# Performance work log

Hardware: AMD Instinct MI355X
Metric: run time of the kernel (lower is better)

The kernel has to match this reference:

```python
import jax, jax.numpy as jnp
import numpy as np

E, K = 8, 2  # num_experts, top_k


def setup_inputs() -> dict:
    key = jax.random.key(0)
    ks = jax.random.split(key, 5)
    B, S, H, I = 2, 1024, 1024, 4096
    scale_h = 1.0 / np.sqrt(H)
    scale_i = 1.0 / np.sqrt(I)
    return {
        "hidden_states": jax.random.normal(ks[0], (B, S, H), jnp.float32),
        "conf_w": jax.random.normal(ks[1], (E, H), jnp.float32) * 0.1 * scale_h,
        "conf_b": jnp.zeros((E,), jnp.float32),
        "gate_w": jax.random.normal(ks[2], (E, I, H), jnp.float32) * scale_h,
        "up_w": jax.random.normal(ks[3], (E, I, H), jnp.float32) * scale_h,
        "down_w": jax.random.normal(ks[4], (E, H, I), jnp.float32) * scale_i,
        "wealth": jnp.ones((E,), jnp.float32),
    }


def reference(hidden_states, conf_w, conf_b, gate_w, up_w, down_w, wealth):
    x = hidden_states  # (B,S,H)
    # Per-expert confidence heads: sigmoid(Linear(H->1)) stacked -> (B,S,E)
    confidences = jax.nn.sigmoid(jnp.einsum("bsh,eh->bse", x, conf_w) + conf_b)
    # VCG auction: bid = confidence * wealth
    bids = confidences * wealth  # (B,S,E)
    top_bids, selected_experts = jax.lax.top_k(bids, K)  # (B,S,K)
    # payments = (K+1)-th highest bid (unused in output but part of forward math)
    sorted_bids = -jnp.sort(-bids, axis=-1)
    payments = jnp.broadcast_to(sorted_bids[..., K:K + 1], top_bids.shape)
    routing_weights = jax.nn.softmax(top_bids, axis=-1)  # (B,S,K)
    # combine weights per expert: sum_k rw_k * [sel_k == e] -> (B,S,E)
    combine = jnp.sum(
        jax.nn.one_hot(selected_experts, E, dtype=x.dtype)
        * routing_weights[..., None],
        axis=2,
    )

    def ffn(gw, uw, dw):
        # SwiGLU expert: down(silu(gate(x)) * up(x))
        g = jnp.einsum("bsh,ih->bsi", x, gw)
        u = jnp.einsum("bsh,ih->bsi", x, uw)
        return jnp.einsum("bsi,hi->bsh", jax.nn.silu(g) * u, dw)

    expert_out = jax.vmap(ffn)(gate_w, up_w, down_w)  # (E,B,S,H)
    output = jnp.einsum("ebsh,bse->bsh", expert_out, combine)
    return output
```

## Files before the change

### kernel.cpp

```cpp
#include <hip/hip_runtime.h>
#include <math.h>

#define NEXP 8
#define TILE 128
#define BK 32

typedef __attribute__((ext_vector_type(8))) short short8;
typedef __attribute__((ext_vector_type(4))) float float4v;

__device__ __forceinline__ unsigned short f2bf(float f) {
  union { float f; unsigned u; } v; v.f = f;
  unsigned r = v.u + 0x7FFFu + ((v.u >> 16) & 1u);
  return (unsigned short)(r >> 16);
}
__device__ __forceinline__ unsigned pack2(float a, float b) {
  return (unsigned)f2bf(a) | ((unsigned)f2bf(b) << 16);
}

__device__ __forceinline__ void gll16(const void* g, void* l) {
  __builtin_amdgcn_global_load_lds(
      (const __attribute__((address_space(1))) unsigned int*)(unsigned long long)(uintptr_t)g,
      (__attribute__((address_space(3))) unsigned int*)(unsigned)(uintptr_t)l,
      16, 0, 0);
}

__global__ __launch_bounds__(256) void convert_x_kernel(
    const float* __restrict__ x, unsigned short* __restrict__ xb, int n4) {
  int i = blockIdx.x * 256 + threadIdx.x;
  if (i >= n4) return;
  float4 v = ((const float4*)x)[i];
  uint2 o; o.x = pack2(v.x, v.y); o.y = pack2(v.z, v.w);
  ((uint2*)xb)[i] = o;
}

__global__ __launch_bounds__(256) void pack_w_kernel(
    const float* __restrict__ src, unsigned short* __restrict__ dst, int K) {
  const int ks = blockIdx.x, rt = blockIdx.y, e = blockIdx.z;
  const int n_ks = gridDim.x, n_rt = gridDim.y;
  const int r = threadIdx.x >> 1, half = threadIdx.x & 1;
  const size_t R = (size_t)n_rt * TILE;
  const float4* s = (const float4*)(src + ((size_t)e * R + rt * TILE + r) * K + ks * BK + half * 16);
  float4 v0 = s[0], v1 = s[1], v2 = s[2], v3 = s[3];
  uint4 o0, o1;
  o0.x = pack2(v0.x, v0.y); o0.y = pack2(v0.z, v0.w);
  o0.z = pack2(v1.x, v1.y); o0.w = pack2(v1.z, v1.w);
  o1.x = pack2(v2.x, v2.y); o1.y = pack2(v2.z, v2.w);
  o1.z = pack2(v3.x, v3.y); o1.w = pack2(v3.z, v3.w);
  unsigned short* pb = dst + ((size_t)(e * n_rt + rt) * n_ks + ks) * (TILE * BK)
                           + (r >> 4) * 512 + (r & 15) * 8;
  *(uint4*)(pb + (2 * half) * 128)     = o0;
  *(uint4*)(pb + (2 * half + 1) * 128) = o1;
}

__global__ __launch_bounds__(256) void routing_kernel(
    const float* __restrict__ x, const float* __restrict__ cw,
    const float* __restrict__ cb, const float* __restrict__ wealth,
    int* __restrict__ plist, int* __restrict__ counts,
    float* __restrict__ w_rt, int T, int H) {
  const int t = blockIdx.x;
  const int tid = threadIdx.x;
  const float* xr = x + (size_t)t * H;
  float acc[NEXP];
#pragma unroll
  for (int e = 0; e < NEXP; ++e) acc[e] = 0.f;
  for (int h = tid; h < H; h += 256) {
    float xv = xr[h];
#pragma unroll
    for (int e = 0; e < NEXP; ++e) acc[e] += xv * cw[e * H + h];
  }
  __shared__ float s[NEXP][256];
#pragma unroll
  for (int e = 0; e < NEXP; ++e) s[e][tid] = acc[e];
  __syncthreads();
  for (int st = 128; st > 0; st >>= 1) {
    if (tid < st) {
#pragma unroll
      for (int e = 0; e < NEXP; ++e) s[e][tid] += s[e][tid + st];
    }
    __syncthreads();
  }
  if (tid == 0) {
    float bids[NEXP];
#pragma unroll
    for (int e = 0; e < NEXP; ++e) {
      float lg = s[e][0] + cb[e];
      float c = 1.f / (1.f + expf(-lg));
      bids[e] = c * wealth[e];
    }
    int i0 = 0;
    for (int e = 1; e < NEXP; ++e) if (bids[e] > bids[i0]) i0 = e;
    int i1 = (i0 == 0) ? 1 : 0;
    for (int e = 0; e < NEXP; ++e) if (e != i0 && bids[e] > bids[i1]) i1 = e;
    float ex = expf(bids[i1] - bids[i0]);
    float wsum = 1.f + ex;
    w_rt[2 * t]     = 1.f / wsum;
    w_rt[2 * t + 1] = ex / wsum;
    int p0 = atomicAdd(&counts[i0], 1);
    plist[i0 * T + p0] = 2 * t;
    int p1 = atomicAdd(&counts[i1], 1);
    plist[i1 * T + p1] = 2 * t + 1;
  }
}

__global__ __launch_bounds__(256, 2) void gateup_kernel(
    const unsigned short* __restrict__ xb, const unsigned short* __restrict__ gwp,
    const unsigned short* __restrict__ uwp, const int* __restrict__ plist,
    const int* __restrict__ counts, unsigned short* __restrict__ act,
    int T, int H, int I) {
  const int nx = gridDim.x, ny = gridDim.y, nz = gridDim.z;
  int rt = blockIdx.x, it = blockIdx.y, e = blockIdx.z;
  {
    int nwg = nx * ny * nz;
    if (((nwg & 7) == 0) && (((nwg >> 3) % nx) == 0)) {
      int orig = blockIdx.x + nx * (blockIdx.y + ny * blockIdx.z);
      int idx = orig >> 3, xcd = orig & 7;
      int q = idx / nx;
      rt = idx - q * nx;
      int chunk = q * 8 + xcd;
      it = chunk % ny;
      e = chunk / ny;
    }
  }
  const int cnt = counts[e];
  const int row0 = rt * TILE;
  if (row0 >= cnt) return;
  const int nks = H / BK;

  __shared__ __align__(16) unsigned short As[2][TILE * BK];
  __shared__ __align__(16) unsigned short Bg[2][TILE * BK];
  __shared__ __align__(16) unsigned short Bu[2][TILE * BK];

  const int tid = threadIdx.x, lane = tid & 63, wv = tid >> 6;
  const int wm = wv >> 1, wn = wv & 1;
  const int quad = lane >> 4, l15 = lane & 15;

  int ri0 = row0 + wv * 32 + l15;
  int ri1 = ri0 + 16;
  if (ri0 >= cnt) ri0 = cnt - 1;
  if (ri1 >= cnt) ri1 = cnt - 1;
  const unsigned short* a0 = xb + (size_t)(plist[e * T + ri0] >> 1) * H + quad * 8;
  const unsigned short* a1 = xb + (size_t)(plist[e * T + ri1] >> 1) * H + quad * 8;

  const size_t pan = ((size_t)(e * ny + it) * nks) * (TILE * BK);
  const unsigned short* g0 = gwp + pan + (size_t)wv * 1024 + (size_t)lane * 8;
  const unsigned short* u0 = uwp + pan + (size_t)wv * 1024 + (size_t)lane * 8;

  float4v accg[4][4], accu[4][4];
#pragma unroll
  for (int a = 0; a < 4; ++a)
#pragma unroll
    for (int b = 0; b < 4; ++b) {
      float4v z = {0.f, 0.f, 0.f, 0.f};
      accg[a][b] = z; accu[a][b] = z;
    }

  auto stage = [&](int kk, int b) {
    unsigned short* lA = &As[b][wv * 1024];
    unsigned short* lG = &Bg[b][wv * 1024];
    unsigned short* lU = &Bu[b][wv * 1024];
    size_t ka = (size_t)kk * BK;
    size_t kb = (size_t)kk * (TILE * BK);
    gll16(a0 + ka, lA);       gll16(a1 + ka, lA + 512);
    gll16(g0 + kb, lG);       gll16(g0 + kb + 512, lG + 512);
    gll16(u0 + kb, lU);       gll16(u0 + kb + 512, lU + 512);
  };

  stage(0, 0);
  __syncthreads();
  for (int k = 0; k < nks; ++k) {
    const int cb = k & 1;
    if (k + 1 < nks) stage(k + 1, cb ^ 1);
    short8 af[4], bgf[4], buf_[4];
#pragma unroll
    for (int mi = 0; mi < 4; ++mi)
      af[mi] = *(const short8*)(&As[cb][(wm * 4 + mi) * 512 + quad * 128 + l15 * 8]);
#pragma unroll
    for (int ni = 0; ni < 4; ++ni) {
      bgf[ni]  = *(const short8*)(&Bg[cb][(wn * 4 + ni) * 512 + quad * 128 + l15 * 8]);
      buf_[ni] = *(const short8*)(&Bu[cb][(wn * 4 + ni) * 512 + quad * 128 + l15 * 8]);
    }
#pragma unroll
    for (int mi = 0; mi < 4; ++mi)
#pragma unroll
      for (int ni = 0; ni < 4; ++ni) {
        accg[mi][ni] = __builtin_amdgcn_mfma_f32_16x16x32_bf16(af[mi], bgf[ni], accg[mi][ni], 0, 0, 0);
        accu[mi][ni] = __builtin_amdgcn_mfma_f32_16x16x32_bf16(af[mi], buf_[ni], accu[mi][ni], 0, 0, 0);
      }
    __syncthreads();
  }

#pragma unroll
  for (int mi = 0; mi < 4; ++mi) {
    int rbase = wm * 64 + mi * 16 + quad * 4;
#pragma unroll
    for (int r = 0; r < 4; ++r) {
      int grow = row0 + rbase + r;
      if (grow < cnt) {
        int p = plist[e * T + grow];
        size_t base = (size_t)p * I + it * TILE + wn * 64 + l15;
#pragma unroll
        for (int ni = 0; ni < 4; ++ni) {
          float g = accg[mi][ni][r];
          float u = accu[mi][ni][r];
          float s = g / (1.f + __expf(-g)) * u;
          act[base + ni * 16] = f2bf(s);
        }
      }
    }
  }
}

__global__ __launch_bounds__(256, 2) void down_kernel(
    const unsigned short* __restrict__ act, const unsigned short* __restrict__ dwp,
    const int* __restrict__ plist, const int* __restrict__ counts,
    float* __restrict__ part, int T, int H, int I) {
  const int nx = gridDim.x, ny = gridDim.y, nz = gridDim.z;
  int rt = blockIdx.x, ht = blockIdx.y, zz = blockIdx.z;
  {
    int nwg = nx * ny * nz;
    if (((nwg & 7) == 0) && (((nwg >> 3) % nx) == 0)) {
      int orig = blockIdx.x + nx * (blockIdx.y + ny * blockIdx.z);
      int idx = orig >> 3, xcd = orig & 7;
      int q = idx / nx;
      rt = idx - q * nx;
      int chunk = q * 8 + xcd;
      ht = chunk % ny;
      zz = chunk / ny;
    }
  }
  const int e = zz >> 1, split = zz & 1;
  const int cnt = counts[e];
  const int row0 = rt * TILE;
  if (row0 >= cnt) return;
  const int nks_tot = I / BK;
  const int nks = nks_tot >> 1;
  const int k0 = split * nks;

  __shared__ __align__(16) unsigned short As[2][TILE * BK];
  __shared__ __align__(16) unsigned short Bs[2][TILE * BK];

  const int tid = threadIdx.x, lane = tid & 63, wv = tid >> 6;
  const int wm = wv >> 1, wn = wv & 1;
  const int quad = lane >> 4, l15 = lane & 15;

  int ri0 = row0 + wv * 32 + l15;
  int ri1 = ri0 + 16;
  if (ri0 >= cnt) ri0 = cnt - 1;
  if (ri1 >= cnt) ri1 = cnt - 1;
  const unsigned short* a0 = act + (size_t)plist[e * T + ri0] * I + k0 * BK + quad * 8;
  const unsigned short* a1 = act + (size_t)plist[e * T + ri1] * I + k0 * BK + quad * 8;

  const size_t pan = ((size_t)(e * ny + ht) * nks_tot + k0) * (TILE * BK);
  const unsigned short* b0 = dwp + pan + (size_t)wv * 1024 + (size_t)lane * 8;

  float4v acc[4][4];
#pragma unroll
  for (int a = 0; a < 4; ++a)
#pragma unroll
    for (int b = 0; b < 4; ++b) { float4v z = {0.f, 0.f, 0.f, 0.f}; acc[a][b] = z; }

  auto stage = [&](int kk, int b) {
    unsigned short* lA = &As[b][wv * 1024];
    unsigned short* lB = &Bs[b][wv * 1024];
    size_t ka = (size_t)kk * BK;
    size_t kb = (size_t)kk * (TILE * BK);
    gll16(a0 + ka, lA);  gll16(a1 + ka, lA + 512);
    gll16(b0 + kb, lB);  gll16(b0 + kb + 512, lB + 512);
  };

  stage(0, 0);
  __syncthreads();
  for (int k = 0; k < nks; ++k) {
    const int cb = k & 1;
    if (k + 1 < nks) stage(k + 1, cb ^ 1);
    short8 af[4], bf[4];
#pragma unroll
    for (int mi = 0; mi < 4; ++mi)
      af[mi] = *(const short8*)(&As[cb][(wm * 4 + mi) * 512 + quad * 128 + l15 * 8]);
#pragma unroll
    for (int ni = 0; ni < 4; ++ni)
      bf[ni] = *(const short8*)(&Bs[cb][(wn * 4 + ni) * 512 + quad * 128 + l15 * 8]);
#pragma unroll
    for (int mi = 0; mi < 4; ++mi)
#pragma unroll
      for (int ni = 0; ni < 4; ++ni)
        acc[mi][ni] = __builtin_amdgcn_mfma_f32_16x16x32_bf16(af[mi], bf[ni], acc[mi][ni], 0, 0, 0);
    __syncthreads();
  }

#pragma unroll
  for (int mi = 0; mi < 4; ++mi) {
    int rbase = wm * 64 + mi * 16 + quad * 4;
#pragma unroll
    for (int r = 0; r < 4; ++r) {
      int grow = row0 + rbase + r;
      if (grow < cnt) {
        int p = plist[e * T + grow];
        size_t base = ((size_t)split * 2 * T + p) * H + ht * TILE + wn * 64 + l15;
#pragma unroll
        for (int ni = 0; ni < 4; ++ni)
          part[base + ni * 16] = acc[mi][ni][r];
      }
    }
  }
}

__global__ __launch_bounds__(256) void combine_kernel(
    const float* __restrict__ part, const float* __restrict__ w_rt,
    float* __restrict__ out, int T, int H) {
  int h4 = H >> 2;
  int n4 = T * h4;
  int i = blockIdx.x * 256 + threadIdx.x;
  if (i >= n4) return;
  int t = i / h4;
  int c = i - t * h4;
  float w0 = w_rt[2 * t], w1 = w_rt[2 * t + 1];
  size_t splitoff = (size_t)2 * T * H / 4;
  const float4* pa = (const float4*)(part + (size_t)(2 * t) * H);
  const float4* pb = (const float4*)(part + (size_t)(2 * t + 1) * H);
  float4 a0 = pa[c], a1 = pa[c + splitoff];
  float4 b0 = pb[c], b1 = pb[c + splitoff];
  float4 o;
  o.x = w0 * (a0.x + a1.x) + w1 * (b0.x + b1.x);
  o.y = w0 * (a0.y + a1.y) + w1 * (b0.y + b1.y);
  o.z = w0 * (a0.z + a1.z) + w1 * (b0.z + b1.z);
  o.w = w0 * (a0.w + a1.w) + w1 * (b0.w + b1.w);
  ((float4*)(out + (size_t)t * H))[c] = o;
}

extern "C" void kernel_launch(void* const* d_in, const int* in_sizes, int n_in,
                              void* d_out, int out_size, void* d_ws, size_t ws_size,
                              hipStream_t stream) {
  const float* x      = (const float*)d_in[0];
  const float* cw     = (const float*)d_in[1];
  const float* cb     = (const float*)d_in[2];
  const float* gw     = (const float*)d_in[3];
  const float* uw     = (const float*)d_in[4];
  const float* dw     = (const float*)d_in[5];
  const float* wealth = (const float*)d_in[6];
  float* out = (float*)d_out;

  const int H = in_sizes[1] / NEXP;
  const int T = in_sizes[0] / H;
  const int I = in_sizes[3] / (NEXP * H);

  char* ws = (char*)d_ws;
  size_t off = 0;
  unsigned short* xb  = (unsigned short*)(ws + off); off += (size_t)T * H * 2;
  unsigned short* act = (unsigned short*)(ws + off); off += (size_t)2 * T * I * 2;
  float* part = (float*)(ws + off); off += (size_t)2 * 2 * T * H * 4;
  unsigned short* gwp = (unsigned short*)(ws + off); off += (size_t)NEXP * I * H * 2;
  unsigned short* uwp = (unsigned short*)(ws + off); off += (size_t)NEXP * I * H * 2;
  unsigned short* dwp = gwp;
  int* plist = (int*)(ws + off); off += (size_t)NEXP * T * 4;
  float* w_rt = (float*)(ws + off); off += (size_t)T * 2 * 4;
  int* counts = (int*)(ws + off); off += NEXP * 4;

  hipMemsetAsync(counts, 0, NEXP * sizeof(int), stream);

  int n4 = (T * H) / 4;
  convert_x_kernel<<<(n4 + 255) / 256, 256, 0, stream>>>(x, xb, n4);
  routing_kernel<<<T, 256, 0, stream>>>(x, cw, cb, wealth, plist, counts, w_rt, T, H);

  dim3 gp(H / BK, I / TILE, NEXP);
  pack_w_kernel<<<gp, 256, 0, stream>>>(gw, gwp, H);
  pack_w_kernel<<<gp, 256, 0, stream>>>(uw, uwp, H);

  int ttiles = (T + TILE - 1) / TILE;
  dim3 g1(ttiles, I / TILE, NEXP);
  gateup_kernel<<<g1, 256, 0, stream>>>(xb, gwp, uwp, plist, counts, act, T, H, I);

  dim3 gpd(I / BK, H / TILE, NEXP);
  pack_w_kernel<<<gpd, 256, 0, stream>>>(dw, dwp, I);

  dim3 g2(ttiles, H / TILE, NEXP * 2);
  down_kernel<<<g2, 256, 0, stream>>>(act, dwp, plist, counts, part, T, H, I);

  combine_kernel<<<(n4 + 255) / 256, 256, 0, stream>>>(part, w_rt, out, T, H);
}
```

Baseline: 692.6 us.

## Fuse fp32 weight conversion into GEMM loads and merge routing with x conversion

Removes the separate weight pack kernels. The gate/up and down GEMMs now read fp32 weights directly into registers, convert them with v_cvt_pk_bf16_f32, and write them into LDS in the MFMA layout, with the register prefetch overlapping the MFMA work. The x conversion and the routing are merged into one launch, and routing uses one wave per token with shuffle reductions. The gain is fewer passes over the weights and fewer launches. In exchange each GEMM tile re-reads fp32 weights (twice the bytes) once per token tile, adds register pressure, and down_kernel's launch bound rises to 3 blocks.

```diff
diff --git a/kernel.cpp b/kernel.cpp
--- a/kernel.cpp
+++ b/kernel.cpp
@@ -15,6 +15,17 @@
 }
 __device__ __forceinline__ unsigned pack2(float a, float b) {
   return (unsigned)f2bf(a) | ((unsigned)f2bf(b) << 16);
+}
+__device__ __forceinline__ unsigned cvtpk(float lo, float hi) {
+  unsigned r;
+  asm("v_cvt_pk_bf16_f32 %0, %1, %2" : "=v"(r) : "v"(lo), "v"(hi));
+  return r;
+}
+__device__ __forceinline__ uint4 cvt8(float4 a, float4 b) {
+  uint4 o;
+  o.x = cvtpk(a.x, a.y); o.y = cvtpk(a.z, a.w);
+  o.z = cvtpk(b.x, b.y); o.w = cvtpk(b.z, b.w);
+  return o;
 }
 
 __device__ __forceinline__ void gll16(const void* g, void* l) {
@@ -24,66 +35,51 @@
       16, 0, 0);
 }
 
-__global__ __launch_bounds__(256) void convert_x_kernel(
-    const float* __restrict__ x, unsigned short* __restrict__ xb, int n4) {
-  int i = blockIdx.x * 256 + threadIdx.x;
-  if (i >= n4) return;
-  float4 v = ((const float4*)x)[i];
-  uint2 o; o.x = pack2(v.x, v.y); o.y = pack2(v.z, v.w);
-  ((uint2*)xb)[i] = o;
-}
-
-__global__ __launch_bounds__(256) void pack_w_kernel(
-    const float* __restrict__ src, unsigned short* __restrict__ dst, int K) {
-  const int ks = blockIdx.x, rt = blockIdx.y, e = blockIdx.z;
-  const int n_ks = gridDim.x, n_rt = gridDim.y;
-  const int r = threadIdx.x >> 1, half = threadIdx.x & 1;
-  const size_t R = (size_t)n_rt * TILE;
-  const float4* s = (const float4*)(src + ((size_t)e * R + rt * TILE + r) * K + ks * BK + half * 16);
-  float4 v0 = s[0], v1 = s[1], v2 = s[2], v3 = s[3];
-  uint4 o0, o1;
-  o0.x = pack2(v0.x, v0.y); o0.y = pack2(v0.z, v0.w);
-  o0.z = pack2(v1.x, v1.y); o0.w = pack2(v1.z, v1.w);
-  o1.x = pack2(v2.x, v2.y); o1.y = pack2(v2.z, v2.w);
-  o1.z = pack2(v3.x, v3.y); o1.w = pack2(v3.z, v3.w);
-  unsigned short* pb = dst + ((size_t)(e * n_rt + rt) * n_ks + ks) * (TILE * BK)
-                           + (r >> 4) * 512 + (r & 15) * 8;
-  *(uint4*)(pb + (2 * half) * 128)     = o0;
-  *(uint4*)(pb + (2 * half + 1) * 128) = o1;
-}
-
-__global__ __launch_bounds__(256) void routing_kernel(
+__global__ __launch_bounds__(256) void prep_kernel(
     const float* __restrict__ x, const float* __restrict__ cw,
     const float* __restrict__ cb, const float* __restrict__ wealth,
-    int* __restrict__ plist, int* __restrict__ counts,
-    float* __restrict__ w_rt, int T, int H) {
-  const int t = blockIdx.x;
-  const int tid = threadIdx.x;
-  const float* xr = x + (size_t)t * H;
+    unsigned short* __restrict__ xb, int* __restrict__ plist,
+    int* __restrict__ counts, float* __restrict__ w_rt,
+    int T, int H, int n4, int nconv) {
+  const int b = blockIdx.x;
+  if (b < nconv) {
+    int i = b * 256 + threadIdx.x;
+    if (i < n4) {
+      float4 v = ((const float4*)x)[i];
+      uint2 o; o.x = pack2(v.x, v.y); o.y = pack2(v.z, v.w);
+      ((uint2*)xb)[i] = o;
+    }
+    return;
+  }
+  int t = (b - nconv) * 4 + (threadIdx.x >> 6);
+  if (t >= T) return;
+  const int lane = threadIdx.x & 63;
+  const float4* x4 = (const float4*)(x + (size_t)t * H);
+  const float4* c4 = (const float4*)cw;
+  const int h4n = H >> 2;
   float acc[NEXP];
 #pragma unroll
   for (int e = 0; e < NEXP; ++e) acc[e] = 0.f;
-  for (int h = tid; h < H; h += 256) {
-    float xv = xr[h];
-#pragma unroll
-    for (int e = 0; e < NEXP; ++e) acc[e] += xv * cw[e * H + h];
-  }
-  __shared__ float s[NEXP][256];
-#pragma unroll
-  for (int e = 0; e < NEXP; ++e) s[e][tid] = acc[e];
-  __syncthreads();
-  for (int st = 128; st > 0; st >>= 1) {
-    if (tid < st) {
-#pragma unroll
-      for (int e = 0; e < NEXP; ++e) s[e][tid] += s[e][tid + st];
-    }
-    __syncthreads();
-  }
-  if (tid == 0) {
+  for (int h = lane; h < h4n; h += 64) {
+    float4 xv = x4[h];
+#pragma unroll
+    for (int e = 0; e < NEXP; ++e) {
+      float4 cv = c4[(size_t)e * h4n + h];
+      acc[e] += xv.x * cv.x + xv.y * cv.y + xv.z * cv.z + xv.w * cv.w;
+    }
+  }
+#pragma unroll
+  for (int e = 0; e < NEXP; ++e) {
+    float v = acc[e];
+#pragma unroll
+    for (int off = 32; off > 0; off >>= 1) v += __shfl_down(v, off, 64);
+    acc[e] = v;
+  }
+  if (lane == 0) {
     float bids[NEXP];
 #pragma unroll
     for (int e = 0; e < NEXP; ++e) {
-      float lg = s[e][0] + cb[e];
+      float lg = acc[e] + cb[e];
       float c = 1.f / (1.f + expf(-lg));
       bids[e] = c * wealth[e];
     }
@@ -103,8 +99,8 @@
 }
 
 __global__ __launch_bounds__(256, 2) void gateup_kernel(
-    const unsigned short* __restrict__ xb, const unsigned short* __restrict__ gwp,
-    const unsigned short* __restrict__ uwp, const int* __restrict__ plist,
+    const unsigned short* __restrict__ xb, const float* __restrict__ gw,
+    const float* __restrict__ uw, const int* __restrict__ plist,
     const int* __restrict__ counts, unsigned short* __restrict__ act,
     int T, int H, int I) {
   const int nx = gridDim.x, ny = gridDim.y, nz = gridDim.z;
@@ -141,9 +137,11 @@
   const unsigned short* a0 = xb + (size_t)(plist[e * T + ri0] >> 1) * H + quad * 8;
   const unsigned short* a1 = xb + (size_t)(plist[e * T + ri1] >> 1) * H + quad * 8;
 
-  const size_t pan = ((size_t)(e * ny + it) * nks) * (TILE * BK);
-  const unsigned short* g0 = gwp + pan + (size_t)wv * 1024 + (size_t)lane * 8;
-  const unsigned short* u0 = uwp + pan + (size_t)wv * 1024 + (size_t)lane * 8;
+  const int brow = wv * 32 + (lane >> 1);
+  const int bhalf = lane & 1;
+  const float* gsrc = gw + ((size_t)e * I + (size_t)it * TILE + brow) * H + bhalf * 16;
+  const float* usrc = uw + ((size_t)e * I + (size_t)it * TILE + brow) * H + bhalf * 16;
+  const int woff = (brow >> 4) * 512 + bhalf * 256 + (brow & 15) * 8;
 
   float4v accg[4][4], accu[4][4];
 #pragma unroll
@@ -154,22 +152,34 @@
       accg[a][b] = z; accu[a][b] = z;
     }
 
-  auto stage = [&](int kk, int b) {
-    unsigned short* lA = &As[b][wv * 1024];
-    unsigned short* lG = &Bg[b][wv * 1024];
-    unsigned short* lU = &Bu[b][wv * 1024];
-    size_t ka = (size_t)kk * BK;
-    size_t kb = (size_t)kk * (TILE * BK);
-    gll16(a0 + ka, lA);       gll16(a1 + ka, lA + 512);
-    gll16(g0 + kb, lG);       gll16(g0 + kb + 512, lG + 512);
-    gll16(u0 + kb, lU);       gll16(u0 + kb + 512, lU + 512);
-  };
-
-  stage(0, 0);
+  float4 gr0, gr1, gr2, gr3, ur0, ur1, ur2, ur3;
+  auto loadB = [&](int kk) {
+    const float4* gs = (const float4*)(gsrc + (size_t)kk * BK);
+    const float4* us = (const float4*)(usrc + (size_t)kk * BK);
+    gr0 = gs[0]; gr1 = gs[1]; gr2 = gs[2]; gr3 = gs[3];
+    ur0 = us[0]; ur1 = us[1]; ur2 = us[2]; ur3 = us[3];
+  };
+  auto writeB = [&](int b) {
+    uint4 q0 = cvt8(gr0, gr1), q1 = cvt8(gr2, gr3);
+    uint4 q2 = cvt8(ur0, ur1), q3 = cvt8(ur2, ur3);
+    *(uint4*)(&Bg[b][woff])       = q0;
+    *(uint4*)(&Bg[b][woff + 128]) = q1;
+    *(uint4*)(&Bu[b][woff])       = q2;
+    *(uint4*)(&Bu[b][woff + 128]) = q3;
+  };
+  auto stageA = [&](int kk, int b) {
+    gll16(a0 + (size_t)kk * BK, &As[b][wv * 1024]);
+    gll16(a1 + (size_t)kk * BK, &As[b][wv * 1024 + 512]);
+  };
+
+  loadB(0);
+  stageA(0, 0);
+  writeB(0);
   __syncthreads();
+
   for (int k = 0; k < nks; ++k) {
     const int cb = k & 1;
-    if (k + 1 < nks) stage(k + 1, cb ^ 1);
+    if (k + 1 < nks) { loadB(k + 1); stageA(k + 1, cb ^ 1); }
     short8 af[4], bgf[4], buf_[4];
 #pragma unroll
     for (int mi = 0; mi < 4; ++mi)
@@ -186,6 +196,7 @@
         accg[mi][ni] = __builtin_amdgcn_mfma_f32_16x16x32_bf16(af[mi], bgf[ni], accg[mi][ni], 0, 0, 0);
         accu[mi][ni] = __builtin_amdgcn_mfma_f32_16x16x32_bf16(af[mi], buf_[ni], accu[mi][ni], 0, 0, 0);
       }
+    if (k + 1 < nks) writeB(cb ^ 1);
     __syncthreads();
   }
 
@@ -210,8 +221,8 @@
   }
 }
 
-__global__ __launch_bounds__(256, 2) void down_kernel(
-    const unsigned short* __restrict__ act, const unsigned short* __restrict__ dwp,
+__global__ __launch_bounds__(256, 3) void down_kernel(
+    const unsigned short* __restrict__ act, const float* __restrict__ dw,
     const int* __restrict__ plist, const int* __restrict__ counts,
     float* __restrict__ part, int T, int H, int I) {
   const int nx = gridDim.x, ny = gridDim.y, nz = gridDim.z;
@@ -250,8 +261,10 @@
   const unsigned short* a0 = act + (size_t)plist[e * T + ri0] * I + k0 * BK + quad * 8;
   const unsigned short* a1 = act + (size_t)plist[e * T + ri1] * I + k0 * BK + quad * 8;
 
-  const size_t pan = ((size_t)(e * ny + ht) * nks_tot + k0) * (TILE * BK);
-  const unsigned short* b0 = dwp + pan + (size_t)wv * 1024 + (size_t)lane * 8;
+  const int brow = wv * 32 + (lane >> 1);
+  const int bhalf = lane & 1;
+  const float* dsrc = dw + ((size_t)e * H + (size_t)ht * TILE + brow) * I + k0 * BK + bhalf * 16;
+  const int woff = (brow >> 4) * 512 + bhalf * 256 + (brow & 15) * 8;
 
   float4v acc[4][4];
 #pragma unroll
@@ -259,20 +272,29 @@
 #pragma unroll
     for (int b = 0; b < 4; ++b) { float4v z = {0.f, 0.f, 0.f, 0.f}; acc[a][b] = z; }
 
-  auto stage = [&](int kk, int b) {
-    unsigned short* lA = &As[b][wv * 1024];
-    unsigned short* lB = &Bs[b][wv * 1024];
-    size_t ka = (size_t)kk * BK;
-    size_t kb = (size_t)kk * (TILE * BK);
-    gll16(a0 + ka, lA);  gll16(a1 + ka, lA + 512);
-    gll16(b0 + kb, lB);  gll16(b0 + kb + 512, lB + 512);
-  };
-
-  stage(0, 0);
+  float4 dr0, dr1, dr2, dr3;
+  auto loadB = [&](int kk) {
+    const float4* ds = (const float4*)(dsrc + (size_t)kk * BK);
+    dr0 = ds[0]; dr1 = ds[1]; dr2 = ds[2]; dr3 = ds[3];
+  };
+  auto writeB = [&](int b) {
+    uint4 q0 = cvt8(dr0, dr1), q1 = cvt8(dr2, dr3);
+    *(uint4*)(&Bs[b][woff])       = q0;
+    *(uint4*)(&Bs[b][woff + 128]) = q1;
+  };
+  auto stageA = [&](int kk, int b) {
+    gll16(a0 + (size_t)kk * BK, &As[b][wv * 1024]);
+    gll16(a1 + (size_t)kk * BK, &As[b][wv * 1024 + 512]);
+  };
+
+  loadB(0);
+  stageA(0, 0);
+  writeB(0);
   __syncthreads();
+
   for (int k = 0; k < nks; ++k) {
     const int cb = k & 1;
-    if (k + 1 < nks) stage(k + 1, cb ^ 1);
+    if (k + 1 < nks) { loadB(k + 1); stageA(k + 1, cb ^ 1); }
     short8 af[4], bf[4];
 #pragma unroll
     for (int mi = 0; mi < 4; ++mi)
@@ -285,6 +307,7 @@
 #pragma unroll
       for (int ni = 0; ni < 4; ++ni)
         acc[mi][ni] = __builtin_amdgcn_mfma_f32_16x16x32_bf16(af[mi], bf[ni], acc[mi][ni], 0, 0, 0);
+    if (k + 1 < nks) writeB(cb ^ 1);
     __syncthreads();
   }
 
@@ -349,9 +372,6 @@
   unsigned short* xb  = (unsigned short*)(ws + off); off += (size_t)T * H * 2;
   unsigned short* act = (unsigned short*)(ws + off); off += (size_t)2 * T * I * 2;
   float* part = (float*)(ws + off); off += (size_t)2 * 2 * T * H * 4;
-  unsigned short* gwp = (unsigned short*)(ws + off); off += (size_t)NEXP * I * H * 2;
-  unsigned short* uwp = (unsigned short*)(ws + off); off += (size_t)NEXP * I * H * 2;
-  unsigned short* dwp = gwp;
   int* plist = (int*)(ws + off); off += (size_t)NEXP * T * 4;
   float* w_rt = (float*)(ws + off); off += (size_t)T * 2 * 4;
   int* counts = (int*)(ws + off); off += NEXP * 4;
@@ -359,22 +379,17 @@
   hipMemsetAsync(counts, 0, NEXP * sizeof(int), stream);
 
   int n4 = (T * H) / 4;
-  convert_x_kernel<<<(n4 + 255) / 256, 256, 0, stream>>>(x, xb, n4);
-  routing_kernel<<<T, 256, 0, stream>>>(x, cw, cb, wealth, plist, counts, w_rt, T, H);
-
-  dim3 gp(H / BK, I / TILE, NEXP);
-  pack_w_kernel<<<gp, 256, 0, stream>>>(gw, gwp, H);
-  pack_w_kernel<<<gp, 256, 0, stream>>>(uw, uwp, H);
+  int nconv = (n4 + 255) / 256;
+  int nrout = (T + 3) / 4;
+  prep_kernel<<<nconv + nrout, 256, 0, stream>>>(x, cw, cb, wealth, xb, plist,
+                                                 counts, w_rt, T, H, n4, nconv);
 
   int ttiles = (T + TILE - 1) / TILE;
   dim3 g1(ttiles, I / TILE, NEXP);
-  gateup_kernel<<<g1, 256, 0, stream>>>(xb, gwp, uwp, plist, counts, act, T, H, I);
-
-  dim3 gpd(I / BK, H / TILE, NEXP);
-  pack_w_kernel<<<gpd, 256, 0, stream>>>(dw, dwp, I);
+  gateup_kernel<<<g1, 256, 0, stream>>>(xb, gw, uw, plist, counts, act, T, H, I);
 
   dim3 g2(ttiles, H / TILE, NEXP * 2);
-  down_kernel<<<g2, 256, 0, stream>>>(act, dwp, plist, counts, part, T, H, I);
+  down_kernel<<<g2, 256, 0, stream>>>(act, dw, plist, counts, part, T, H, I);
 
   combine_kernel<<<(n4 + 255) / 256, 256, 0, stream>>>(part, w_rt, out, T, H);
 }
```

After: 679.7 us. Within noise of the previous version (-1.9%).

## Fuse weight packing, x conversion and routing into one prep kernel

Applied to the files above, without the earlier changes.

Merges the gate/up/down weight bf16 packing, x conversion and routing into a single heterogeneous prep launch. Each packing block now processes a large slab, and routing uses one wavefront per token with float4 loads and shuffle reductions. Down weights get their own workspace buffer when it fits, so they can be packed up front instead of after gate/up. This cuts launch count and serialization, at the cost of needing more workspace and uneven work per block within one grid.

```diff
diff --git a/kernel.cpp b/kernel.cpp
--- a/kernel.cpp
+++ b/kernel.cpp
@@ -24,66 +24,91 @@
       16, 0, 0);
 }
 
-__global__ __launch_bounds__(256) void convert_x_kernel(
-    const float* __restrict__ x, unsigned short* __restrict__ xb, int n4) {
-  int i = blockIdx.x * 256 + threadIdx.x;
-  if (i >= n4) return;
-  float4 v = ((const float4*)x)[i];
-  uint2 o; o.x = pack2(v.x, v.y); o.y = pack2(v.z, v.w);
-  ((uint2*)xb)[i] = o;
-}
-
-__global__ __launch_bounds__(256) void pack_w_kernel(
-    const float* __restrict__ src, unsigned short* __restrict__ dst, int K) {
-  const int ks = blockIdx.x, rt = blockIdx.y, e = blockIdx.z;
-  const int n_ks = gridDim.x, n_rt = gridDim.y;
-  const int r = threadIdx.x >> 1, half = threadIdx.x & 1;
-  const size_t R = (size_t)n_rt * TILE;
-  const float4* s = (const float4*)(src + ((size_t)e * R + rt * TILE + r) * K + ks * BK + half * 16);
-  float4 v0 = s[0], v1 = s[1], v2 = s[2], v3 = s[3];
-  uint4 o0, o1;
-  o0.x = pack2(v0.x, v0.y); o0.y = pack2(v0.z, v0.w);
-  o0.z = pack2(v1.x, v1.y); o0.w = pack2(v1.z, v1.w);
-  o1.x = pack2(v2.x, v2.y); o1.y = pack2(v2.z, v2.w);
-  o1.z = pack2(v3.x, v3.y); o1.w = pack2(v3.z, v3.w);
-  unsigned short* pb = dst + ((size_t)(e * n_rt + rt) * n_ks + ks) * (TILE * BK)
-                           + (r >> 4) * 512 + (r & 15) * 8;
-  *(uint4*)(pb + (2 * half) * 128)     = o0;
-  *(uint4*)(pb + (2 * half + 1) * 128) = o1;
-}
-
-__global__ __launch_bounds__(256) void routing_kernel(
-    const float* __restrict__ x, const float* __restrict__ cw,
-    const float* __restrict__ cb, const float* __restrict__ wealth,
-    int* __restrict__ plist, int* __restrict__ counts,
-    float* __restrict__ w_rt, int T, int H) {
-  const int t = blockIdx.x;
+__device__ __forceinline__ void pack_slab(
+    const float* __restrict__ src, unsigned short* __restrict__ dst,
+    int e, int rt, int cc, int K, int n_rt, int n_ks, int tid) {
+  const int row = tid >> 1, half = tid & 1;
+  const float* sb = src + ((size_t)(e * n_rt + rt) * 128 + row) * K + cc * 1024 + half * 16;
+  unsigned short* db = dst + ((size_t)(e * n_rt + rt) * n_ks + cc * 32) * 4096
+                           + (row >> 4) * 512 + (row & 15) * 8 + half * 256;
+#pragma unroll 4
+  for (int kk = 0; kk < 32; ++kk) {
+    const float4* s = (const float4*)(sb + kk * 32);
+    float4 v0 = s[0], v1 = s[1], v2 = s[2], v3 = s[3];
+    uint4 o0, o1;
+    o0.x = pack2(v0.x, v0.y); o0.y = pack2(v0.z, v0.w);
+    o0.z = pack2(v1.x, v1.y); o0.w = pack2(v1.z, v1.w);
+    o1.x = pack2(v2.x, v2.y); o1.y = pack2(v2.z, v2.w);
+    o1.z = pack2(v3.x, v3.y); o1.w = pack2(v3.z, v3.w);
+    unsigned short* d = db + kk * 4096;
+    *(uint4*)d = o0;
+    *(uint4*)(d + 128) = o1;
+  }
+}
+
+__global__ __launch_bounds__(256) void prep_kernel(
+    const float* __restrict__ gw, const float* __restrict__ uw,
+    const float* __restrict__ dw, const float* __restrict__ x,
+    const float* __restrict__ cw, const float* __restrict__ cbv,
+    const float* __restrict__ wealth,
+    unsigned short* __restrict__ gwp, unsigned short* __restrict__ uwp,
+    unsigned short* __restrict__ dwp, unsigned short* __restrict__ xb,
+    int* __restrict__ plist, int* __restrict__ counts, float* __restrict__ w_rt,
+    int T, int H, int I, int ndw, int nconv, int n4) {
+  const int b = blockIdx.x;
   const int tid = threadIdx.x;
-  const float* xr = x + (size_t)t * H;
+  const int npack = 512 + ndw;
+  if (b < npack) {
+    if (b < 256) {
+      pack_slab(gw, gwp, b >> 5, b & 31, 0, H, 32, 32, tid);
+    } else if (b < 512) {
+      int i = b - 256;
+      pack_slab(uw, uwp, i >> 5, i & 31, 0, H, 32, 32, tid);
+    } else {
+      int i = b - 512;
+      pack_slab(dw, dwp, i >> 5, (i & 31) >> 2, i & 3, I, 8, 128, tid);
+    }
+    return;
+  }
+  if (b < npack + nconv) {
+    int i = (b - npack) * 256 + tid;
+    int stride = nconv * 256;
+    for (; i < n4; i += stride) {
+      float4 v = ((const float4*)x)[i];
+      uint2 o; o.x = pack2(v.x, v.y); o.y = pack2(v.z, v.w);
+      ((uint2*)xb)[i] = o;
+    }
+    return;
+  }
+  int t = (b - npack - nconv) * 4 + (tid >> 6);
+  if (t >= T) return;
+  const int lane = tid & 63;
+  const float4* x4 = (const float4*)(x + (size_t)t * H);
+  const float4* c4 = (const float4*)cw;
+  const int h4n = H >> 2;
   float acc[NEXP];
 #pragma unroll
   for (int e = 0; e < NEXP; ++e) acc[e] = 0.f;
-  for (int h = tid; h < H; h += 256) {
-    float xv = xr[h];
-#pragma unroll
-    for (int e = 0; e < NEXP; ++e) acc[e] += xv * cw[e * H + h];
-  }
-  __shared__ float s[NEXP][256];
-#pragma unroll
-  for (int e = 0; e < NEXP; ++e) s[e][tid] = acc[e];
-  __syncthreads();
-  for (int st = 128; st > 0; st >>= 1) {
-    if (tid < st) {
-#pragma unroll
-      for (int e = 0; e < NEXP; ++e) s[e][tid] += s[e][tid + st];
-    }
-    __syncthreads();
-  }
-  if (tid == 0) {
+  for (int h = lane; h < h4n; h += 64) {
+    float4 xv = x4[h];
+#pragma unroll
+    for (int e = 0; e < NEXP; ++e) {
+      float4 cv = c4[(size_t)e * h4n + h];
+      acc[e] += xv.x * cv.x + xv.y * cv.y + xv.z * cv.z + xv.w * cv.w;
+    }
+  }
+#pragma unroll
+  for (int e = 0; e < NEXP; ++e) {
+    float v = acc[e];
+#pragma unroll
+    for (int off = 32; off > 0; off >>= 1) v += __shfl_down(v, off, 64);
+    acc[e] = v;
+  }
+  if (lane == 0) {
     float bids[NEXP];
 #pragma unroll
     for (int e = 0; e < NEXP; ++e) {
-      float lg = s[e][0] + cb[e];
+      float lg = acc[e] + cbv[e];
       float c = 1.f / (1.f + expf(-lg));
       bids[e] = c * wealth[e];
     }
@@ -100,6 +125,12 @@
     int p1 = atomicAdd(&counts[i1], 1);
     plist[i1 * T + p1] = 2 * t + 1;
   }
+}
+
+__global__ __launch_bounds__(256) void pack_dw_kernel(
+    const float* __restrict__ dw, unsigned short* __restrict__ dwp, int I) {
+  int i = blockIdx.x;
+  pack_slab(dw, dwp, i >> 5, (i & 31) >> 2, i & 3, I, 8, 128, threadIdx.x);
 }
 
 __global__ __launch_bounds__(256, 2) void gateup_kernel(
@@ -351,27 +382,29 @@
   float* part = (float*)(ws + off); off += (size_t)2 * 2 * T * H * 4;
   unsigned short* gwp = (unsigned short*)(ws + off); off += (size_t)NEXP * I * H * 2;
   unsigned short* uwp = (unsigned short*)(ws + off); off += (size_t)NEXP * I * H * 2;
-  unsigned short* dwp = gwp;
   int* plist = (int*)(ws + off); off += (size_t)NEXP * T * 4;
   float* w_rt = (float*)(ws + off); off += (size_t)T * 2 * 4;
   int* counts = (int*)(ws + off); off += NEXP * 4;
+  size_t dwp_need = off + (size_t)NEXP * H * I * 2;
+  int sep = (ws_size >= dwp_need) ? 1 : 0;
+  unsigned short* dwp = sep ? (unsigned short*)(ws + off) : gwp;
 
   hipMemsetAsync(counts, 0, NEXP * sizeof(int), stream);
 
   int n4 = (T * H) / 4;
-  convert_x_kernel<<<(n4 + 255) / 256, 256, 0, stream>>>(x, xb, n4);
-  routing_kernel<<<T, 256, 0, stream>>>(x, cw, cb, wealth, plist, counts, w_rt, T, H);
-
-  dim3 gp(H / BK, I / TILE, NEXP);
-  pack_w_kernel<<<gp, 256, 0, stream>>>(gw, gwp, H);
-  pack_w_kernel<<<gp, 256, 0, stream>>>(uw, uwp, H);
+  int nconv = 256;
+  int nrout = (T + 3) / 4;
+  int ndw = sep ? 256 : 0;
+  int nprep = 512 + ndw + nconv + nrout;
+  prep_kernel<<<nprep, 256, 0, stream>>>(gw, uw, dw, x, cw, cb, wealth,
+                                         gwp, uwp, dwp, xb, plist, counts, w_rt,
+                                         T, H, I, ndw, nconv, n4);
 
   int ttiles = (T + TILE - 1) / TILE;
   dim3 g1(ttiles, I / TILE, NEXP);
   gateup_kernel<<<g1, 256, 0, stream>>>(xb, gwp, uwp, plist, counts, act, T, H, I);
 
-  dim3 gpd(I / BK, H / TILE, NEXP);
-  pack_w_kernel<<<gpd, 256, 0, stream>>>(dw, dwp, I);
+  if (!sep) pack_dw_kernel<<<256, 256, 0, stream>>>(dw, dwp, I);
 
   dim3 g2(ttiles, H / TILE, NEXP * 2);
   down_kernel<<<g2, 256, 0, stream>>>(act, dwp, plist, counts, part, T, H, I);
```

Result: no change. 690.8 us (-0.3%).
